# Kernel tuning notes

Hardware: AMD Instinct MI355X
Metric: run time of the kernel (lower is better)

## Reference

```python
import jax, jax.numpy as jnp
import numpy as np

N_VERTS = 100000
N_JOINTS = 24
N_BETAS = 10
N_POSEDIRS = 207  # (24-1)*9
# Standard SMPL kinematic tree parents
PARENTS = np.array([-1, 0, 0, 0, 1, 2, 3, 4, 5, 6, 7, 8, 9, 9, 9, 12, 13, 14, 16, 17, 18, 19, 20, 21])


def setup_inputs() -> dict:
    key = jax.random.key(0)
    ks = jax.random.split(key, 9)
    f = jnp.float32
    return {
        "betas": jax.random.normal(ks[0], (N_BETAS,), f),
        "pose": jax.random.normal(ks[1], (N_JOINTS, 3), f) * 0.2,
        "scale": jnp.ones((1,), f),
        "trans": jax.random.normal(ks[2], (3,), f),
        "v_template": jax.random.normal(ks[3], (N_VERTS, 3), f),
        "shapedirs": jax.random.normal(ks[4], (N_VERTS, 3, N_BETAS), f) * 0.01,
        "posedirs": jax.random.normal(ks[5], (N_VERTS, 3, N_POSEDIRS), f) * 0.01,
        "J_regressor": jax.random.uniform(ks[6], (N_JOINTS, N_VERTS), f) / N_VERTS,
        "weights": jax.nn.softmax(jax.random.normal(ks[7], (N_VERTS, N_JOINTS), f), axis=-1),
    }


def rodrigues(r):
    """Axis-angle [J,3] -> rotation matrices [J,3,3] (matches torch impl; eps kept tiny+deterministic)."""
    theta = jnp.linalg.norm(r + 1e-8, axis=-1, keepdims=True)  # [J,1]
    r_hat = r / theta
    z = jnp.zeros_like(r_hat[:, 0])
    K = jnp.stack([z, -r_hat[:, 2], r_hat[:, 1],
                   r_hat[:, 2], z, -r_hat[:, 0],
                   -r_hat[:, 1], r_hat[:, 0], z], axis=1).reshape(-1, 3, 3)
    c = jnp.cos(theta)[..., None]  # [J,1,1]
    s = jnp.sin(theta)[..., None]
    outer = r_hat[:, :, None] * r_hat[:, None, :]  # [J,3,3]
    I = jnp.eye(3, dtype=r.dtype)
    return c * I + (1.0 - c) * outer + s * K


def reference(betas, pose, scale, trans, v_template, shapedirs, posedirs, J_regressor, weights):
    dt = v_template.dtype
    # blend shapes
    v_shaped = jnp.einsum('vks,s->vk', shapedirs, betas) + v_template  # [V,3]
    J = J_regressor @ v_shaped  # [24,3]
    R = rodrigues(pose)  # [24,3,3]
    I3 = jnp.eye(3, dtype=dt)
    lrotmin = (R[1:] - I3).reshape(-1)  # [207]
    v_posed = v_shaped + jnp.einsum('vkp,p->vk', posedirs, lrotmin)  # [V,3]
    # forward kinematics over 24-joint chain
    bottom = jnp.array([[0.0, 0.0, 0.0, 1.0]], dtype=dt)
    def make_A(Ri, t):
        return jnp.concatenate([jnp.concatenate([Ri, t[:, None]], axis=1), bottom], axis=0)  # [4,4]
    As = [make_A(R[0], J[0])]
    for i in range(1, N_JOINTS):
        p = int(PARENTS[i])
        As.append(As[p] @ make_A(R[i], J[i] - J[p]))
    G = jnp.stack(As)  # [24,4,4]
    # remove rest-pose joint locations
    Jh = jnp.concatenate([J, jnp.zeros((N_JOINTS, 1), dt)], axis=1)  # [24,4]
    corr = jnp.einsum('jab,jb->ja', G, Jh)  # [24,4]
    rel = G - jnp.concatenate([jnp.zeros((N_JOINTS, 4, 3), dt), corr[:, :, None]], axis=2)
    # linear blend skinning
    T = jnp.einsum('vj,jab->vab', weights, rel)  # [V,4,4]
    vh = jnp.concatenate([v_posed, jnp.ones((v_posed.shape[0], 1), dt)], axis=1)  # [V,4]
    v = jnp.einsum('vab,vb->va', T, vh)[:, :3]  # [V,3]
    return v * scale.reshape(()) + trans[None, :]
```

## Files before the change

### kernel.cpp

```cpp
#include <hip/hip_runtime.h>

#define NV 100000
#define NJ 24
#define NP 207
#define NPART 25
#define VPB 8
#define NTILES (NV / VPB)
#define TF4 1242
#define GRIDF 1024

__global__ __launch_bounds__(256) void k_shape(
    const float* __restrict__ betas, const float* __restrict__ v_template,
    const float* __restrict__ shapedirs, float* __restrict__ v_shaped) {
  __shared__ float sb[10];
  if (threadIdx.x < 10) sb[threadIdx.x] = betas[threadIdx.x];
  __syncthreads();
  int t = blockIdx.x * 256 + threadIdx.x;
  if (t >= 3 * NV / 2) return;
  const float4* sd4 = (const float4*)(shapedirs + (size_t)t * 20);
  float4 f0 = sd4[0], f1 = sd4[1], f2 = sd4[2], f3 = sd4[3], f4v = sd4[4];
  float2 vt = ((const float2*)v_template)[t];
  float a = vt.x
          + f0.x * sb[0] + f0.y * sb[1] + f0.z * sb[2] + f0.w * sb[3]
          + f1.x * sb[4] + f1.y * sb[5] + f1.z * sb[6] + f1.w * sb[7]
          + f2.x * sb[8] + f2.y * sb[9];
  float b = vt.y
          + f2.z * sb[0] + f2.w * sb[1]
          + f3.x * sb[2] + f3.y * sb[3] + f3.z * sb[4] + f3.w * sb[5]
          + f4v.x * sb[6] + f4v.y * sb[7] + f4v.z * sb[8] + f4v.w * sb[9];
  ((float2*)v_shaped)[t] = make_float2(a, b);
}

__global__ __launch_bounds__(256) void k_jreg(
    const float* __restrict__ Jreg, const float* __restrict__ v_shaped,
    float* __restrict__ jpT) {
  int j = blockIdx.x, part = blockIdx.y, tid = threadIdx.x;
  const int SL = NV / NPART;
  int v0 = part * SL;
  const float4* w4 = (const float4*)(Jreg + (size_t)j * NV + v0);
  const float4* s4 = (const float4*)(v_shaped + (size_t)3 * v0);
  float s0 = 0.f, s1 = 0.f, s2 = 0.f;
  for (int i4 = tid; i4 < SL / 4; i4 += 256) {
    float4 w = w4[i4];
    float4 A = s4[3 * i4 + 0];
    float4 B = s4[3 * i4 + 1];
    float4 C = s4[3 * i4 + 2];
    s0 += w.x * A.x + w.y * A.w + w.z * B.z + w.w * C.y;
    s1 += w.x * A.y + w.y * B.x + w.z * B.w + w.w * C.z;
    s2 += w.x * A.z + w.y * B.y + w.z * C.x + w.w * C.w;
  }
  __shared__ float red[256][3];
  red[tid][0] = s0; red[tid][1] = s1; red[tid][2] = s2;
  __syncthreads();
  for (int off = 128; off > 0; off >>= 1) {
    if (tid < off) {
      red[tid][0] += red[tid + off][0];
      red[tid][1] += red[tid + off][1];
      red[tid][2] += red[tid + off][2];
    }
    __syncthreads();
  }
  if (tid < 3) jpT[(j * 3 + tid) * 32 + part] = red[0][tid];
}

__device__ __forceinline__ void stage_tile(float4* dst, const float4* src, int tid) {
  #pragma unroll
  for (int r = 0; r < 5; ++r) {
    int i4 = r * 256 + tid;
    if (i4 < TF4) {
      __builtin_amdgcn_global_load_lds(
          (const __attribute__((address_space(1))) void*)(src + i4),
          (__attribute__((address_space(3))) void*)(dst + r * 256 + (tid & 192)),
          16, 0, 0);
    }
  }
}

__global__ __launch_bounds__(256, 4) void k_fused(
    const float* __restrict__ posedirs, const float* __restrict__ wgt,
    const float* __restrict__ pose, const float* __restrict__ jpT,
    const float* __restrict__ scale, const float* __restrict__ trans,
    float* __restrict__ vbuf) {
  __shared__ float4 tile[2][TF4];
  int tid = threadIdx.x, b = blockIdx.x;
  int wid = tid >> 6, lane = tid & 63, half = lane >> 5, lj = lane & 31;
  const float4* pd4 = (const float4*)posedirs;

  int vv0 = b * VPB + (wid << 1) + half;
  float pvl = (lj < 3) ? vbuf[(size_t)3 * vv0 + lj] : 0.f;
  float wj  = (lj < NJ) ? wgt[(size_t)vv0 * NJ + lj] : 0.f;
  __builtin_amdgcn_sched_barrier(0);
  stage_tile(&tile[0][0], pd4 + (size_t)b * TF4, tid);

  float* fkJ  = (float*)&tile[1][0];
  float* fkR  = fkJ + 72;
  float* fkG  = fkJ + 288;
  float* lrs  = fkJ + 576;
  float* relS = fkJ + 784;
  if (tid < NJ * 3) {
    const float* src = jpT + tid * 32;
    float a = 0.f;
    #pragma unroll
    for (int i = 0; i < NPART; ++i) a += src[i];
    fkJ[tid] = a;
  }
  if (tid < NJ) {
    float rx = pose[tid * 3 + 0], ry = pose[tid * 3 + 1], rz = pose[tid * 3 + 2];
    float tx = rx + 1e-8f, ty = ry + 1e-8f, tz = rz + 1e-8f;
    float theta = sqrtf(tx * tx + ty * ty + tz * tz);
    float x = rx / theta, y = ry / theta, z = rz / theta;
    float c = cosf(theta), s = sinf(theta), C = 1.f - c;
    float Rr[9];
    Rr[0] = c + C * x * x;     Rr[1] = C * x * y - s * z; Rr[2] = C * x * z + s * y;
    Rr[3] = C * x * y + s * z; Rr[4] = c + C * y * y;     Rr[5] = C * y * z - s * x;
    Rr[6] = C * x * z - s * y; Rr[7] = C * y * z + s * x; Rr[8] = c + C * z * z;
    #pragma unroll
    for (int e = 0; e < 9; ++e) fkR[tid * 9 + e] = Rr[e];
    if (tid >= 1) {
      #pragma unroll
      for (int e = 0; e < 9; ++e) {
        float id = (e == 0 || e == 4 || e == 8) ? 1.f : 0.f;
        lrs[(tid - 1) * 9 + e] = Rr[e] - id;
      }
    }
  }
  __syncthreads();
  if (tid < 3) {
    const int par[NJ] = {-1,0,0,0,1,2,3,4,5,6,7,8,9,9,9,12,13,14,16,17,18,19,20,21};
    int a = tid;
    fkG[a * 4 + 0] = fkR[a * 3 + 0];
    fkG[a * 4 + 1] = fkR[a * 3 + 1];
    fkG[a * 4 + 2] = fkR[a * 3 + 2];
    fkG[a * 4 + 3] = fkJ[a];
    #pragma unroll
    for (int i = 1; i < NJ; ++i) {
      int p = par[i];
      float t0 = fkJ[i * 3 + 0] - fkJ[p * 3 + 0];
      float t1 = fkJ[i * 3 + 1] - fkJ[p * 3 + 1];
      float t2 = fkJ[i * 3 + 2] - fkJ[p * 3 + 2];
      float g0 = fkG[p * 12 + a * 4 + 0], g1 = fkG[p * 12 + a * 4 + 1];
      float g2 = fkG[p * 12 + a * 4 + 2], g3 = fkG[p * 12 + a * 4 + 3];
      fkG[i * 12 + a * 4 + 0] = g0 * fkR[i * 9 + 0] + g1 * fkR[i * 9 + 3] + g2 * fkR[i * 9 + 6];
      fkG[i * 12 + a * 4 + 1] = g0 * fkR[i * 9 + 1] + g1 * fkR[i * 9 + 4] + g2 * fkR[i * 9 + 7];
      fkG[i * 12 + a * 4 + 2] = g0 * fkR[i * 9 + 2] + g1 * fkR[i * 9 + 5] + g2 * fkR[i * 9 + 8];
      fkG[i * 12 + a * 4 + 3] = g3 + g0 * t0 + g1 * t1 + g2 * t2;
    }
  }
  __syncthreads();
  if (tid < NJ) {
    #pragma unroll
    for (int a = 0; a < 3; ++a) {
      float corr = fkG[tid * 12 + a * 4 + 0] * fkJ[tid * 3 + 0] +
                   fkG[tid * 12 + a * 4 + 1] * fkJ[tid * 3 + 1] +
                   fkG[tid * 12 + a * 4 + 2] * fkJ[tid * 3 + 2];
      relS[tid * 12 + a * 4 + 0] = fkG[tid * 12 + a * 4 + 0];
      relS[tid * 12 + a * 4 + 1] = fkG[tid * 12 + a * 4 + 1];
      relS[tid * 12 + a * 4 + 2] = fkG[tid * 12 + a * 4 + 2];
      relS[tid * 12 + a * 4 + 3] = fkG[tid * 12 + a * 4 + 3] - corr;
    }
  }
  __syncthreads();

  float llr[7];
  #pragma unroll
  for (int e = 0; e < 7; ++e) {
    int p = lj + 32 * e;
    llr[e] = (p < NP) ? lrs[p] : 0.f;
  }
  float rlq[12];
  #pragma unroll
  for (int e = 0; e < 12; ++e) rlq[e] = (lj < NJ) ? relS[lj * 12 + e] : 0.f;
  float sc = scale[0];
  float tr = (lj < 3) ? trans[lj] : 0.f;

  int nt = (NTILES - 1 - b) / GRIDF + 1;
  __syncthreads();

  for (int it = 0; it < nt; ++it) {
    int cur = it & 1;
    int tnE = b + (it + 1) * GRIDF;
    if (tnE >= NTILES) tnE = NTILES - 1;
    int vvn = tnE * VPB + (wid << 1) + half;
    float pvl_n = (lj < 3) ? vbuf[(size_t)3 * vvn + lj] : 0.f;
    float wj_n  = (lj < NJ) ? wgt[(size_t)vvn * NJ + lj] : 0.f;
    __builtin_amdgcn_sched_barrier(0);
    stage_tile(&tile[cur ^ 1][0], pd4 + (size_t)tnE * TF4, tid);
    asm volatile("s_waitcnt vmcnt(7)" ::: "memory");
    __builtin_amdgcn_sched_barrier(0);
    __builtin_amdgcn_s_barrier();
    __builtin_amdgcn_sched_barrier(0);

    int vv = (b + it * GRIDF) * VPB + (wid << 1) + half;
    const float* row = (const float*)&tile[cur][0] + ((wid << 1) + half) * (3 * NP);
    float a0 = 0.f, a1 = 0.f, a2 = 0.f;
    #pragma unroll
    for (int e = 0; e < 7; ++e) {
      int p = lj + 32 * e;
      if (p < NP) {
        float l = llr[e];
        a0 += row[p] * l;
        a1 += row[NP + p] * l;
        a2 += row[2 * NP + p] * l;
      }
    }
    #pragma unroll
    for (int off = 16; off > 0; off >>= 1) {
      a0 += __shfl_xor(a0, off);
      a1 += __shfl_xor(a1, off);
      a2 += __shfl_xor(a2, off);
    }
    int gb = lane & 32;
    float p0 = __shfl(pvl, gb + 0) + a0;
    float p1 = __shfl(pvl, gb + 1) + a1;
    float p2 = __shfl(pvl, gb + 2) + a2;
    float q0 = rlq[0] * p0 + rlq[1] * p1 + rlq[2]  * p2 + rlq[3];
    float q1 = rlq[4] * p0 + rlq[5] * p1 + rlq[6]  * p2 + rlq[7];
    float q2 = rlq[8] * p0 + rlq[9] * p1 + rlq[10] * p2 + rlq[11];
    float r0 = wj * q0, r1 = wj * q1, r2 = wj * q2;
    #pragma unroll
    for (int off = 16; off > 0; off >>= 1) {
      r0 += __shfl_xor(r0, off);
      r1 += __shfl_xor(r1, off);
      r2 += __shfl_xor(r2, off);
    }
    if (lj < 3) {
      float oo = (lj == 0) ? r0 : (lj == 1) ? r1 : r2;
      vbuf[(size_t)3 * vv + lj] = oo * sc + tr;
    }
    __builtin_amdgcn_sched_barrier(0);
    __builtin_amdgcn_s_barrier();
    __builtin_amdgcn_sched_barrier(0);

    pvl = pvl_n; wj = wj_n;
  }
  asm volatile("s_waitcnt vmcnt(0)" ::: "memory");
}

extern "C" void kernel_launch(void* const* d_in, const int* in_sizes, int n_in,
                              void* d_out, int out_size, void* d_ws, size_t ws_size,
                              hipStream_t stream) {
  const float* betas      = (const float*)d_in[0];
  const float* pose       = (const float*)d_in[1];
  const float* scale      = (const float*)d_in[2];
  const float* trans      = (const float*)d_in[3];
  const float* v_template = (const float*)d_in[4];
  const float* shapedirs  = (const float*)d_in[5];
  const float* posedirs   = (const float*)d_in[6];
  const float* Jreg       = (const float*)d_in[7];
  const float* weights    = (const float*)d_in[8];
  float* out = (float*)d_out;
  float* ws  = (float*)d_ws;

  float* jpT = ws;

  k_shape<<<(3 * NV / 2 + 255) / 256, 256, 0, stream>>>(betas, v_template, shapedirs, out);
  k_jreg<<<dim3(NJ, NPART), 256, 0, stream>>>(Jreg, out, jpT);
  k_fused<<<GRIDF, 256, 0, stream>>>(posedirs, weights, pose, jpT, scale, trans, out);
}
```

Measured before the change: 61.62 us.

## Give each wave its own double-buffered posedirs quad and drop block barriers

New measurement: 60.36 us. -2.1%, faster.

```diff
diff --git a/kernel.cpp b/kernel.cpp
--- a/kernel.cpp
+++ b/kernel.cpp
@@ -4,10 +4,9 @@
 #define NJ 24
 #define NP 207
 #define NPART 25
-#define VPB 8
-#define NTILES (NV / VPB)
-#define TF4 1242
-#define GRIDF 1024
+#define NQUADS (NV / 4)
+#define GRIDF 512
+#define NWV (GRIDF * 4)
 
 __global__ __launch_bounds__(256) void k_shape(
     const float* __restrict__ betas, const float* __restrict__ v_template,
@@ -63,36 +62,38 @@
   if (tid < 3) jpT[(j * 3 + tid) * 32 + part] = red[0][tid];
 }
 
-__device__ __forceinline__ void stage_tile(float4* dst, const float4* src, int tid) {
+__device__ __forceinline__ void stage_quad(float4* dst, const float4* src, int lane) {
   #pragma unroll
-  for (int r = 0; r < 5; ++r) {
-    int i4 = r * 256 + tid;
-    if (i4 < TF4) {
-      __builtin_amdgcn_global_load_lds(
-          (const __attribute__((address_space(1))) void*)(src + i4),
-          (__attribute__((address_space(3))) void*)(dst + r * 256 + (tid & 192)),
-          16, 0, 0);
-    }
-  }
-}
-
-__global__ __launch_bounds__(256, 4) void k_fused(
+  for (int r = 0; r < 10; ++r) {
+    int i4 = r * 64 + lane;
+    int i4c = (i4 < 621) ? i4 : 620;
+    __builtin_amdgcn_global_load_lds(
+        (const __attribute__((address_space(1))) void*)(src + i4c),
+        (__attribute__((address_space(3))) void*)(dst + r * 64),
+        16, 0, 0);
+  }
+}
+
+__global__ __launch_bounds__(256, 2) void k_fused(
     const float* __restrict__ posedirs, const float* __restrict__ wgt,
     const float* __restrict__ pose, const float* __restrict__ jpT,
     const float* __restrict__ scale, const float* __restrict__ trans,
     float* __restrict__ vbuf) {
-  __shared__ float4 tile[2][TF4];
+  __shared__ float4 buf[4][2][640];
   int tid = threadIdx.x, b = blockIdx.x;
   int wid = tid >> 6, lane = tid & 63, half = lane >> 5, lj = lane & 31;
+  int W = b * 4 + wid;
   const float4* pd4 = (const float4*)posedirs;
 
-  int vv0 = b * VPB + (wid << 1) + half;
-  float pvl = (lj < 3) ? vbuf[(size_t)3 * vv0 + lj] : 0.f;
-  float wj  = (lj < NJ) ? wgt[(size_t)vv0 * NJ + lj] : 0.f;
+  int q0 = W;
+  float pvl0 = (lj < 3) ? vbuf[(size_t)3 * (q0 * 4 + half) + lj] : 0.f;
+  float wj0  = (lj < NJ) ? wgt[(size_t)(q0 * 4 + half) * NJ + lj] : 0.f;
+  float pvl1 = (lj < 3) ? vbuf[(size_t)3 * (q0 * 4 + 2 + half) + lj] : 0.f;
+  float wj1  = (lj < NJ) ? wgt[(size_t)(q0 * 4 + 2 + half) * NJ + lj] : 0.f;
   __builtin_amdgcn_sched_barrier(0);
-  stage_tile(&tile[0][0], pd4 + (size_t)b * TF4, tid);
-
-  float* fkJ  = (float*)&tile[1][0];
+  stage_quad(&buf[wid][0][0], pd4 + (size_t)q0 * 621, lane);
+
+  float* fkJ  = (float*)&buf[0][1][0];
   float* fkR  = fkJ + 72;
   float* fkG  = fkJ + 288;
   float* lrs  = fkJ + 576;
@@ -173,65 +174,68 @@
   float sc = scale[0];
   float tr = (lj < 3) ? trans[lj] : 0.f;
 
-  int nt = (NTILES - 1 - b) / GRIDF + 1;
-  __syncthreads();
-
+  __syncthreads();
+  asm volatile("s_waitcnt vmcnt(0)" ::: "memory");
+
+  int nt = (NQUADS - 1 - W) / NWV + 1;
   for (int it = 0; it < nt; ++it) {
     int cur = it & 1;
-    int tnE = b + (it + 1) * GRIDF;
-    if (tnE >= NTILES) tnE = NTILES - 1;
-    int vvn = tnE * VPB + (wid << 1) + half;
-    float pvl_n = (lj < 3) ? vbuf[(size_t)3 * vvn + lj] : 0.f;
-    float wj_n  = (lj < NJ) ? wgt[(size_t)vvn * NJ + lj] : 0.f;
+    int qn = W + (it + 1) * NWV;
+    if (qn >= NQUADS) qn = NQUADS - 1;
+    float pvl0_n = (lj < 3) ? vbuf[(size_t)3 * (qn * 4 + half) + lj] : 0.f;
+    float wj0_n  = (lj < NJ) ? wgt[(size_t)(qn * 4 + half) * NJ + lj] : 0.f;
+    float pvl1_n = (lj < 3) ? vbuf[(size_t)3 * (qn * 4 + 2 + half) + lj] : 0.f;
+    float wj1_n  = (lj < NJ) ? wgt[(size_t)(qn * 4 + 2 + half) * NJ + lj] : 0.f;
     __builtin_amdgcn_sched_barrier(0);
-    stage_tile(&tile[cur ^ 1][0], pd4 + (size_t)tnE * TF4, tid);
-    asm volatile("s_waitcnt vmcnt(7)" ::: "memory");
+    stage_quad(&buf[wid][cur ^ 1][0], pd4 + (size_t)qn * 621, lane);
+    asm volatile("s_waitcnt vmcnt(14)" ::: "memory");
     __builtin_amdgcn_sched_barrier(0);
-    __builtin_amdgcn_s_barrier();
-    __builtin_amdgcn_sched_barrier(0);
-
-    int vv = (b + it * GRIDF) * VPB + (wid << 1) + half;
-    const float* row = (const float*)&tile[cur][0] + ((wid << 1) + half) * (3 * NP);
-    float a0 = 0.f, a1 = 0.f, a2 = 0.f;
-    #pragma unroll
-    for (int e = 0; e < 7; ++e) {
-      int p = lj + 32 * e;
-      if (p < NP) {
-        float l = llr[e];
-        a0 += row[p] * l;
-        a1 += row[NP + p] * l;
-        a2 += row[2 * NP + p] * l;
-      }
-    }
-    #pragma unroll
-    for (int off = 16; off > 0; off >>= 1) {
-      a0 += __shfl_xor(a0, off);
-      a1 += __shfl_xor(a1, off);
-      a2 += __shfl_xor(a2, off);
-    }
-    int gb = lane & 32;
-    float p0 = __shfl(pvl, gb + 0) + a0;
-    float p1 = __shfl(pvl, gb + 1) + a1;
-    float p2 = __shfl(pvl, gb + 2) + a2;
-    float q0 = rlq[0] * p0 + rlq[1] * p1 + rlq[2]  * p2 + rlq[3];
-    float q1 = rlq[4] * p0 + rlq[5] * p1 + rlq[6]  * p2 + rlq[7];
-    float q2 = rlq[8] * p0 + rlq[9] * p1 + rlq[10] * p2 + rlq[11];
-    float r0 = wj * q0, r1 = wj * q1, r2 = wj * q2;
-    #pragma unroll
-    for (int off = 16; off > 0; off >>= 1) {
-      r0 += __shfl_xor(r0, off);
-      r1 += __shfl_xor(r1, off);
-      r2 += __shfl_xor(r2, off);
-    }
-    if (lj < 3) {
-      float oo = (lj == 0) ? r0 : (lj == 1) ? r1 : r2;
-      vbuf[(size_t)3 * vv + lj] = oo * sc + tr;
-    }
-    __builtin_amdgcn_sched_barrier(0);
-    __builtin_amdgcn_s_barrier();
-    __builtin_amdgcn_sched_barrier(0);
-
-    pvl = pvl_n; wj = wj_n;
+
+    int q = W + it * NWV;
+    const float* chunk = (const float*)&buf[wid][cur][0];
+    #pragma unroll
+    for (int h = 0; h < 2; ++h) {
+      int vv = q * 4 + 2 * h + half;
+      const float* row = chunk + (2 * h + half) * (3 * NP);
+      float pvl = h ? pvl1 : pvl0;
+      float wj  = h ? wj1 : wj0;
+      float a0 = 0.f, a1 = 0.f, a2 = 0.f;
+      #pragma unroll
+      for (int e = 0; e < 7; ++e) {
+        int p = lj + 32 * e;
+        if (p < NP) {
+          float l = llr[e];
+          a0 += row[p] * l;
+          a1 += row[NP + p] * l;
+          a2 += row[2 * NP + p] * l;
+        }
+      }
+      #pragma unroll
+      for (int off = 16; off > 0; off >>= 1) {
+        a0 += __shfl_xor(a0, off);
+        a1 += __shfl_xor(a1, off);
+        a2 += __shfl_xor(a2, off);
+      }
+      int gb = lane & 32;
+      float p0 = __shfl(pvl, gb + 0) + a0;
+      float p1 = __shfl(pvl, gb + 1) + a1;
+      float p2 = __shfl(pvl, gb + 2) + a2;
+      float q0v = rlq[0] * p0 + rlq[1] * p1 + rlq[2]  * p2 + rlq[3];
+      float q1v = rlq[4] * p0 + rlq[5] * p1 + rlq[6]  * p2 + rlq[7];
+      float q2v = rlq[8] * p0 + rlq[9] * p1 + rlq[10] * p2 + rlq[11];
+      float r0 = wj * q0v, r1 = wj * q1v, r2 = wj * q2v;
+      #pragma unroll
+      for (int off = 16; off > 0; off >>= 1) {
+        r0 += __shfl_xor(r0, off);
+        r1 += __shfl_xor(r1, off);
+        r2 += __shfl_xor(r2, off);
+      }
+      if (lj < 3) {
+        float oo = (lj == 0) ? r0 : (lj == 1) ? r1 : r2;
+        vbuf[(size_t)3 * vv + lj] = oo * sc + tr;
+      }
+    }
+    pvl0 = pvl0_n; wj0 = wj0_n; pvl1 = pvl1_n; wj1 = wj1_n;
   }
   asm volatile("s_waitcnt vmcnt(0)" ::: "memory");
 }
```
